# Performance work log

Measured on AMD Instinct MI355X. Metric: run time of the kernel, lower is better.

Reference implementation:

```python
import jax, jax.numpy as jnp
import numpy as np

N_NODES = 50000
N_EDGES = 800000
D_IN, D_HID, N_CLS, N_PROT = 128, 256, 16, 512
EPS = 1e-6


def setup_inputs() -> dict:
    key = jax.random.key(0)
    ks = jax.random.split(key, 12)
    s = 0.05
    return {
        "x": jax.random.normal(ks[0], (N_NODES, D_IN), dtype=jnp.float32),
        "edge_index": jax.random.randint(ks[1], (2, N_EDGES), 0, N_NODES, dtype=jnp.int64),
        "prot": jax.random.randint(ks[2], (N_PROT,), 0, N_NODES, dtype=jnp.int64),
        "epoch": 1,
        "W0": jax.random.normal(ks[3], (D_IN, D_HID), dtype=jnp.float32) * s,
        "b0": jnp.zeros((D_HID,), jnp.float32),
        "W1": jax.random.normal(ks[4], (D_HID, D_HID), dtype=jnp.float32) * s,
        "b1": jnp.zeros((D_HID,), jnp.float32),
        "Wl1": jax.random.normal(ks[5], (D_HID, D_HID), dtype=jnp.float32) * s,
        "bl1": jnp.zeros((D_HID,), jnp.float32),
        "Wl2": jax.random.normal(ks[6], (D_HID, N_CLS), dtype=jnp.float32) * s,
        "bl2": jnp.zeros((N_CLS,), jnp.float32),
    }


def _gcn_layer(h, W, b, src, dst, norm, n):
    # PyG GCNConv: h' = scatter_add(norm * (h @ W)[src] -> dst) + b
    m = (h @ W)[src] * norm[:, None]
    return jax.ops.segment_sum(m, dst, num_segments=n) + b


def _forward(x, edge_index, prot, W0, b0, W1, b1, Wl1, bl1, Wl2, bl2):
    n = x.shape[0]
    loops = jnp.arange(n, dtype=edge_index.dtype)
    src = jnp.concatenate([edge_index[0], loops])
    dst = jnp.concatenate([edge_index[1], loops])
    deg = jax.ops.segment_sum(jnp.ones_like(dst, dtype=x.dtype), dst, num_segments=n)
    dis = jax.lax.rsqrt(deg)  # deg >= 1 thanks to self loops
    norm = dis[src] * dis[dst]

    h = jax.nn.relu(_gcn_layer(x, W0, b0, src, dst, norm, n))
    h = _gcn_layer(h, W1, b1, src, dst, norm, n)

    # L2 row-normalize (torch divides by the norm directly)
    qn = jnp.linalg.norm(h, axis=1, keepdims=True)
    h = h / qn

    # relative_rep: cosine similarity of every node to each anchor
    anchors = h[prot]                             # [P, H]
    nx = jnp.linalg.norm(h, axis=1)               # [N]
    na = jnp.linalg.norm(anchors, axis=1)         # [P]
    num = h @ anchors.T                           # [N, P]
    x_rel = num / jnp.maximum(nx[:, None] * na[None, :], EPS)

    # classifier head on prototypes -> out_proto, then composed prediction
    lin = lambda z: jax.nn.relu(z @ Wl1 + bl1) @ Wl2 + bl2
    out_proto = jax.nn.log_softmax(lin(anchors), axis=-1)   # [P, C]
    out = jax.nn.log_softmax(x_rel @ out_proto, axis=-1)    # [N, C]
    return out, x_rel, out_proto


def reference(x, edge_index, prot, epoch, W0, b0, W1, b1, Wl1, bl1, Wl2, bl2):
    # epoch >= first_step_epochs (=0) branch: inference-path composition
    return _forward(x, edge_index, prot, W0, b0, W1, b1, Wl1, bl1, Wl2, bl2)


if __name__ == "__main__":
    out, x_rel, out_proto = reference(**setup_inputs())
    print(out.shape, x_rel.shape, out_proto.shape)
```

## Files before the change

kernel.cpp:

```cpp
#include <hip/hip_runtime.h>
#include <hip/hip_bf16.h>
#include <math.h>

#define NN 50000
#define NP 50048
#define EE 800000
#define DIN 128
#define HID 256
#define NCLS 16
#define NPROT 512

typedef __attribute__((ext_vector_type(8))) short short8;
typedef __attribute__((ext_vector_type(4))) float f32x4;

__device__ inline unsigned short f2b(float f) {
    union { float f; unsigned u; } c; c.f = f;
    unsigned u = c.u;
    unsigned r = (u + 0x7FFFu + ((u >> 16) & 1u)) >> 16;
    return (unsigned short)r;
}
__device__ inline float b2f(unsigned short u) {
    union { unsigned u; float f; } c; c.u = ((unsigned)u) << 16; return c.f;
}

#define GL2LDS16(g, l)                                                              \
    __builtin_amdgcn_global_load_lds(                                               \
        (const __attribute__((address_space(1))) unsigned int*)(g),                 \
        (__attribute__((address_space(3))) unsigned int*)(l), 16, 0, 0)


__global__ __launch_bounds__(256) void k_count(const int* __restrict__ dst, int* __restrict__ cnt, int e) {
    int i = blockIdx.x * 256 + threadIdx.x;
    if (i < e) atomicAdd(&cnt[dst[i]], 1);
}

__global__ __launch_bounds__(256) void k_scan1(const int* __restrict__ cnt, int* __restrict__ excl,
                                               int* __restrict__ bsum, float* __restrict__ dis, int n) {
    __shared__ int s[256];
    int t = threadIdx.x;
    int i = blockIdx.x * 256 + t;
    int v = (i < n) ? cnt[i] : 0;
    if (i < n) dis[i] = rsqrtf((float)v + 1.0f);
    s[t] = v; __syncthreads();
    for (int d = 1; d < 256; d <<= 1) {
        int add = (t >= d) ? s[t - d] : 0;
        __syncthreads();
        s[t] += add;
        __syncthreads();
    }
    if (i < n) excl[i] = s[t] - v;
    if (t == 255) bsum[blockIdx.x] = s[255];
}

__global__ __launch_bounds__(256) void k_scan2(const int* __restrict__ bsum, int* __restrict__ boff, int nb) {
    __shared__ int s[256];
    int t = threadIdx.x;
    int v = (t < nb) ? bsum[t] : 0;
    s[t] = v; __syncthreads();
    for (int d = 1; d < 256; d <<= 1) {
        int add = (t >= d) ? s[t - d] : 0;
        __syncthreads();
        s[t] += add;
        __syncthreads();
    }
    if (t < nb) boff[t] = s[t] - v;
}

__global__ __launch_bounds__(256) void k_scan3(const int* __restrict__ excl, const int* __restrict__ boff,
                                               int* __restrict__ off, int n, int e) {
    int i = blockIdx.x * 256 + threadIdx.x;
    if (i < n) off[i] = excl[i] + boff[blockIdx.x];
    if (i == 0) off[n] = e;
}

__global__ __launch_bounds__(256) void k_fill(const int* __restrict__ src, const int* __restrict__ dst,
                                              const int* __restrict__ off, int* __restrict__ cursor,
                                              const float* __restrict__ dis,
                                              int2* __restrict__ csr_e, int e) {
    int i = blockIdx.x * 256 + threadIdx.x;
    if (i >= e) return;
    int s = src[i], d = dst[i];
    int pos = atomicAdd(&cursor[d], 1);
    csr_e[off[d] + pos] = make_int2(s, __float_as_int(dis[s] * dis[d]));
}


#define CAST_BLKS (NN * DIN / 4 / 256)
#define WT0_BLKS  (DIN * HID / 256)
#define WT1_BLKS  (HID * HID / 256)

__global__ __launch_bounds__(256) void k_prep(const float* __restrict__ x, unsigned short* __restrict__ xb,
                                              const float* __restrict__ W0, unsigned short* __restrict__ Wt0,
                                              const float* __restrict__ W1, unsigned short* __restrict__ Wt1) {
    int b = blockIdx.x, t = threadIdx.x;
    if (b < CAST_BLKS) {
        int i = b * 256 + t;
        float4 v = ((const float4*)x)[i];
        ushort4 o; o.x = f2b(v.x); o.y = f2b(v.y); o.z = f2b(v.z); o.w = f2b(v.w);
        ((ushort4*)xb)[i] = o;
    } else if (b < CAST_BLKS + WT0_BLKS) {
        int i = (b - CAST_BLKS) * 256 + t;
        int k = i / HID, n = i - k * HID;
        Wt0[n * DIN + k] = f2b(W0[(size_t)k * HID + n]);
    } else {
        int i = (b - CAST_BLKS - WT0_BLKS) * 256 + t;
        int k = i / HID, n = i - k * HID;
        Wt1[n * HID + k] = f2b(W1[(size_t)k * HID + n]);
    }
}


__global__ __launch_bounds__(256) void k_gemm_mfma(const unsigned short* __restrict__ A,
                                                   const unsigned short* __restrict__ Bt,
                                                   void* __restrict__ C, int M, int Nc, int K, int mode,
                                                   const float* __restrict__ bias) {
    __shared__ __align__(16) unsigned short As[128 * 32];
    __shared__ __align__(16) unsigned short Bs[128 * 32];
    const int t = threadIdx.x;
    const int lane = t & 63;
    const int quad = lane >> 4;
    const int l16 = lane & 15;
    const int wv = t >> 6;
    const int wm = (wv & 1) * 64, wn = (wv >> 1) * 64;
    const int m0 = blockIdx.y * 128, n0 = blockIdx.x * 128;

    f32x4 acc[4][4];
#pragma unroll
    for (int i = 0; i < 4; ++i)
#pragma unroll
        for (int j = 0; j < 4; ++j)
#pragma unroll
            for (int r = 0; r < 4; ++r) acc[i][j][r] = 0.0f;

    const int sr = t >> 2;
    const int sc = (t & 3) * 8;

    for (int k0 = 0; k0 < K; k0 += 32) {
        GL2LDS16(A + (size_t)(m0 + sr) * K + k0 + sc,       &As[t * 8]);
        GL2LDS16(A + (size_t)(m0 + 64 + sr) * K + k0 + sc,  &As[2048 + t * 8]);
        GL2LDS16(Bt + (size_t)(n0 + sr) * K + k0 + sc,      &Bs[t * 8]);
        GL2LDS16(Bt + (size_t)(n0 + 64 + sr) * K + k0 + sc, &Bs[2048 + t * 8]);
        __syncthreads();
        short8 af[4], bf[4];
#pragma unroll
        for (int i = 0; i < 4; ++i)
            af[i] = *(const short8*)&As[(wm + i * 16 + l16) * 32 + quad * 8];
#pragma unroll
        for (int j = 0; j < 4; ++j)
            bf[j] = *(const short8*)&Bs[(wn + j * 16 + l16) * 32 + quad * 8];
#pragma unroll
        for (int i = 0; i < 4; ++i)
#pragma unroll
            for (int j = 0; j < 4; ++j)
                acc[i][j] = __builtin_amdgcn_mfma_f32_16x16x32_bf16(af[i], bf[j], acc[i][j], 0, 0, 0);
        __syncthreads();
    }

#pragma unroll
    for (int i = 0; i < 4; ++i) {
        int rb = m0 + wm + i * 16 + quad * 4;
#pragma unroll
        for (int j = 0; j < 4; ++j) {
            int col = n0 + wn + j * 16 + l16;
#pragma unroll
            for (int rg = 0; rg < 4; ++rg) {
                int r = rb + rg;
                float v = acc[i][j][rg];
                if (mode == 0) {
                    ((unsigned short*)C)[(size_t)r * Nc + col] = f2b(v);
                } else {
                    v = fmaxf(v + bias[col], 0.0f);
                    ((unsigned short*)C)[(size_t)r * Nc + col] = f2b(v);
                }
            }
        }
    }
}


__global__ __launch_bounds__(256) void k_agg128(const unsigned short* __restrict__ xw, const int* __restrict__ off,
                                                const int2* __restrict__ csr, const float* __restrict__ dis,
                                                unsigned short* __restrict__ out, int n) {
    int node = (blockIdx.x * 256 + threadIdx.x) >> 6;
    int lane = threadIdx.x & 63;
    if (node >= n) return;
    float d = dis[node];
    float w0 = d * d;
    ushort2 u = ((const ushort2*)(xw + (size_t)node * DIN))[lane];
    float a0 = w0 * b2f(u.x), a1 = w0 * b2f(u.y);
    int p = off[node], p1 = off[node + 1];
#define G128(e)                                                           \
    {                                                                     \
        ushort2 v = ((const ushort2*)(xw + (size_t)(e).x * DIN))[lane];   \
        float w = __int_as_float((e).y);                                  \
        a0 = fmaf(w, b2f(v.x), a0); a1 = fmaf(w, b2f(v.y), a1);           \
    }
    for (; p + 3 < p1; p += 4) {
        int2 e0 = csr[p], e1 = csr[p + 1], e2 = csr[p + 2], e3 = csr[p + 3];
        G128(e0) G128(e1) G128(e2) G128(e3)
    }
    for (; p < p1; ++p) { int2 e0 = csr[p]; G128(e0) }
#undef G128
    ushort2 o; o.x = f2b(a0); o.y = f2b(a1);
    ((ushort2*)(out + (size_t)node * DIN))[lane] = o;
}


__global__ __launch_bounds__(256) void k_agg256(const unsigned short* __restrict__ xw, const int* __restrict__ off,
                                                const int2* __restrict__ csr, const float* __restrict__ dis,
                                                const float* __restrict__ bias,
                                                unsigned short* __restrict__ out, float* __restrict__ nx, int n) {
    int node = (blockIdx.x * 256 + threadIdx.x) >> 6;
    int lane = threadIdx.x & 63;
    if (node >= n) return;
    float d = dis[node];
    float w0 = d * d;
    ushort4 u = ((const ushort4*)(xw + (size_t)node * HID))[lane];
    float a0 = w0 * b2f(u.x), a1 = w0 * b2f(u.y), a2 = w0 * b2f(u.z), a3 = w0 * b2f(u.w);
    int p = off[node], p1 = off[node + 1];
#define G256(e)                                                           \
    {                                                                     \
        ushort4 v = ((const ushort4*)(xw + (size_t)(e).x * HID))[lane];   \
        float w = __int_as_float((e).y);                                  \
        a0 = fmaf(w, b2f(v.x), a0); a1 = fmaf(w, b2f(v.y), a1);           \
        a2 = fmaf(w, b2f(v.z), a2); a3 = fmaf(w, b2f(v.w), a3);           \
    }
    for (; p + 3 < p1; p += 4) {
        int2 e0 = csr[p], e1 = csr[p + 1], e2 = csr[p + 2], e3 = csr[p + 3];
        G256(e0) G256(e1) G256(e2) G256(e3)
    }
    for (; p < p1; ++p) { int2 e0 = csr[p]; G256(e0) }
#undef G256
    float4 b = ((const float4*)bias)[lane];
    a0 += b.x; a1 += b.y; a2 += b.z; a3 += b.w;
    float ss = a0 * a0 + a1 * a1 + a2 * a2 + a3 * a3;
    for (int m = 32; m >= 1; m >>= 1) ss += __shfl_xor(ss, m, 64);
    float qn = sqrtf(ss);
    a0 /= qn; a1 /= qn; a2 /= qn; a3 /= qn;
    float s2 = a0 * a0 + a1 * a1 + a2 * a2 + a3 * a3;
    for (int m = 32; m >= 1; m >>= 1) s2 += __shfl_xor(s2, m, 64);
    if (lane == 0) nx[node] = sqrtf(s2);
    ushort4 o; o.x = f2b(a0); o.y = f2b(a1); o.z = f2b(a2); o.w = f2b(a3);
    ((ushort4*)(out + (size_t)node * HID))[lane] = o;
}


__global__ __launch_bounds__(256) void k_gproto(const unsigned short* __restrict__ hb,
                                                const int* __restrict__ prot, const float* __restrict__ nx,
                                                unsigned short* __restrict__ aRb, float* __restrict__ na,
                                                const float* __restrict__ Wl1, const float* __restrict__ bl1,
                                                const float* __restrict__ Wl2, const float* __restrict__ bl2,
                                                float* __restrict__ outp) {
    __shared__ float sa[HID];
    __shared__ float st[HID];
    int row = blockIdx.x, t = threadIdx.x;
    int p = prot[row];
    unsigned short us = hb[(size_t)p * HID + t];
    aRb[(size_t)row * HID + t] = us;
    sa[t] = b2f(us);
    if (t == 0) na[row] = nx[p];
    __syncthreads();
    float acc = bl1[t];
#pragma unroll 8
    for (int k = 0; k < HID; ++k) acc = fmaf(sa[k], Wl1[k * HID + t], acc);
    st[t] = fmaxf(acc, 0.0f);
    __syncthreads();
    if (t < 64) {
        int c = t & 15, ch = t >> 4;
        float z = 0.f;
#pragma unroll 8
        for (int k = ch * 64; k < ch * 64 + 64; ++k) z = fmaf(st[k], Wl2[k * NCLS + c], z);
        z += __shfl_xor(z, 16, 64);
        z += __shfl_xor(z, 32, 64);
        z += bl2[c];
        float m = z;
        for (int d = 8; d >= 1; d >>= 1) m = fmaxf(m, __shfl_xor(m, d, 64));
        float e = expf(z - m);
        float s = e;
        for (int d = 8; d >= 1; d >>= 1) s += __shfl_xor(s, d, 64);
        if (t < 16) outp[row * NCLS + c] = z - m - logf(s);
    }
}


#define XSW(row, cs) (((cs) ^ (((row) & 7) << 3)))
#define NWGX (4 * (NP / 128))

__global__ __launch_bounds__(256, 3) void k_xrel_out(const unsigned short* __restrict__ A,
                                                     const unsigned short* __restrict__ Bt,
                                                     const float* __restrict__ nx, const float* __restrict__ na,
                                                     const float* __restrict__ proto,
                                                     float* __restrict__ xrel, float* __restrict__ opart) {
    __shared__ __align__(16) unsigned short As[128 * 32];
    __shared__ __align__(16) unsigned short Bs[128 * 32];
    __shared__ __align__(16) unsigned short Xs[128 * 128];
    __shared__ __align__(16) unsigned short pTc[16 * 136];

    const int bid = blockIdx.x;
    const int q = NWGX / 8, r = NWGX % 8;
    const int xcd = bid & 7, li = bid >> 3;
    const int wk = (xcd < r ? xcd * (q + 1) : r * (q + 1) + (xcd - r) * q) + li;
    const int m0 = (wk >> 2) * 128;
    const int nc = wk & 3;
    const int n0 = nc * 128;

    const int t = threadIdx.x;
    const int lane = t & 63;
    const int quad = lane >> 4;
    const int l16 = lane & 15;
    const int wv = t >> 6;
    const int wm = (wv & 1) * 64, wn = (wv >> 1) * 64;

    float nxv[4][4];
#pragma unroll
    for (int i = 0; i < 4; ++i)
#pragma unroll
        for (int rg = 0; rg < 4; ++rg) {
            int rr = m0 + wm + i * 16 + quad * 4 + rg;
            nxv[i][rg] = nx[rr < NN ? rr : NN - 1];
        }
    float nav[4];
#pragma unroll
    for (int j = 0; j < 4; ++j) nav[j] = na[n0 + wn + j * 16 + l16];

    const int sr = t >> 2;
    const int sc = (t & 3) * 8;

    f32x4 acc[4][4];
#pragma unroll
    for (int i = 0; i < 4; ++i)
#pragma unroll
        for (int j = 0; j < 4; ++j)
#pragma unroll
            for (int rr = 0; rr < 4; ++rr) acc[i][j][rr] = 0.0f;

    for (int k0 = 0; k0 < HID; k0 += 32) {
        GL2LDS16(A + (size_t)(m0 + sr) * HID + k0 + sc,       &As[t * 8]);
        GL2LDS16(A + (size_t)(m0 + 64 + sr) * HID + k0 + sc,  &As[2048 + t * 8]);
        GL2LDS16(Bt + (size_t)(n0 + sr) * HID + k0 + sc,      &Bs[t * 8]);
        GL2LDS16(Bt + (size_t)(n0 + 64 + sr) * HID + k0 + sc, &Bs[2048 + t * 8]);
        __syncthreads();
        short8 af[4], bf[4];
#pragma unroll
        for (int i = 0; i < 4; ++i)
            af[i] = *(const short8*)&As[(wm + i * 16 + l16) * 32 + quad * 8];
#pragma unroll
        for (int j = 0; j < 4; ++j)
            bf[j] = *(const short8*)&Bs[(wn + j * 16 + l16) * 32 + quad * 8];
#pragma unroll
        for (int i = 0; i < 4; ++i)
#pragma unroll
            for (int j = 0; j < 4; ++j)
                acc[i][j] = __builtin_amdgcn_mfma_f32_16x16x32_bf16(af[i], bf[j], acc[i][j], 0, 0, 0);
        __syncthreads();
    }

    for (int i = t; i < 128 * NCLS; i += 256) {
        int kk = i >> 4, c = i & 15;
        pTc[c * 136 + kk] = f2b(proto[(n0 + kk) * NCLS + c]);
    }

#pragma unroll
    for (int i = 0; i < 4; ++i) {
#pragma unroll
        for (int j = 0; j < 4; ++j) {
            int cl = wn + j * 16 + l16;
#pragma unroll
            for (int rg = 0; rg < 4; ++rg) {
                int row = wm + i * 16 + quad * 4 + rg;
                float s = fmaxf(nxv[i][rg] * nav[j], 1e-6f);
                float v = acc[i][j][rg] * __builtin_amdgcn_rcpf(s);
                Xs[row * 128 + XSW(row, cl)] = f2b(v);
            }
        }
    }
    __syncthreads();

    f32x4 oacc[2];
#pragma unroll
    for (int rr = 0; rr < 4; ++rr) { oacc[0][rr] = 0.0f; oacc[1][rr] = 0.0f; }
#pragma unroll
    for (int ii = 0; ii < 2; ++ii) {
        int rb = wv * 32 + ii * 16;
#pragma unroll
        for (int ks = 0; ks < 4; ++ks) {
            int row = rb + l16;
            short8 af = *(const short8*)&Xs[row * 128 + XSW(row, ks * 32 + quad * 8)];
            short8 pb = *(const short8*)&pTc[l16 * 136 + ks * 32 + quad * 8];
            oacc[ii] = __builtin_amdgcn_mfma_f32_16x16x32_bf16(af, pb, oacc[ii], 0, 0, 0);
        }
    }
#pragma unroll
    for (int ii = 0; ii < 2; ++ii)
#pragma unroll
        for (int rg = 0; rg < 4; ++rg) {
            int lrow = wv * 32 + ii * 16 + quad * 4 + rg;
            opart[((size_t)nc * NP + m0 + lrow) * NCLS + l16] = oacc[ii][rg];
        }

#pragma unroll
    for (int it = 0; it < 8; ++it) {
        int idx = it * 256 + t;
        int row = idx >> 4;
        int c8 = (idx & 15) * 8;
        int rr = m0 + row;
        if (rr < NN) {
            short8 u = *(const short8*)&Xs[row * 128 + XSW(row, c8)];
            float* dst = &xrel[(size_t)rr * NPROT + n0 + c8];
            float4 v0, v1;
            v0.x = b2f((unsigned short)u[0]); v0.y = b2f((unsigned short)u[1]);
            v0.z = b2f((unsigned short)u[2]); v0.w = b2f((unsigned short)u[3]);
            v1.x = b2f((unsigned short)u[4]); v1.y = b2f((unsigned short)u[5]);
            v1.z = b2f((unsigned short)u[6]); v1.w = b2f((unsigned short)u[7]);
            *(float4*)dst = v0;
            *(float4*)(dst + 4) = v1;
        }
    }
}


__global__ __launch_bounds__(256) void k_reduce(const float* __restrict__ opart, float* __restrict__ out) {
    int i = blockIdx.x * 256 + threadIdx.x;
    int row = i >> 4, c = i & 15;
    float z = opart[i] + opart[(size_t)NP * NCLS + i] + opart[(size_t)2 * NP * NCLS + i] +
              opart[(size_t)3 * NP * NCLS + i];
    float mx = z;
    for (int d = 8; d >= 1; d >>= 1) mx = fmaxf(mx, __shfl_xor(mx, d, 64));
    float e = expf(z - mx);
    float s = e;
    for (int d = 8; d >= 1; d >>= 1) s += __shfl_xor(s, d, 64);
    if (row < NN) out[(size_t)row * NCLS + c] = z - mx - logf(s);
}


extern "C" void kernel_launch(void* const* d_in, const int* in_sizes, int n_in,
                              void* d_out, int out_size, void* d_ws, size_t ws_size,
                              hipStream_t stream) {
    const float* x    = (const float*)d_in[0];
    const int*   eidx = (const int*)d_in[1];
    const int*   prot = (const int*)d_in[2];
    const float* W0  = (const float*)d_in[4];
    const float* b0  = (const float*)d_in[5];
    const float* W1  = (const float*)d_in[6];
    const float* b1  = (const float*)d_in[7];
    const float* Wl1 = (const float*)d_in[8];
    const float* bl1 = (const float*)d_in[9];
    const float* Wl2 = (const float*)d_in[10];
    const float* bl2 = (const float*)d_in[11];

    const int N = NN, E = EE;
    const int* esrc_in = eidx;
    const int* edst_in = eidx + E;

    float* out_final = (float*)d_out;
    float* x_rel     = (float*)d_out + (size_t)N * NCLS;
    float* out_proto = x_rel + (size_t)N * NPROT;

    char* w = (char*)d_ws;
    auto alloc = [&](size_t bytes) { char* p = w; w += (bytes + 255) & ~(size_t)255; return p; };
    int*   cnt      = (int*)alloc((size_t)N * 4);
    int*   cursor   = (int*)alloc((size_t)N * 4);
    float* dis      = (float*)alloc((size_t)N * 4);
    int*   excl     = (int*)alloc((size_t)N * 4);
    int*   csr_off  = (int*)alloc((size_t)(N + 1) * 4);
    int*   bsum     = (int*)alloc(1024);
    int*   boff     = (int*)alloc(1024);
    int2*  csr_e    = (int2*)alloc((size_t)E * 8);
    float* nx       = (float*)alloc((size_t)N * 4);
    float* na       = (float*)alloc((size_t)NPROT * 4);
    float* opart    = (float*)alloc((size_t)4 * NP * NCLS * 4);
    unsigned short* xb    = (unsigned short*)alloc((size_t)NP * DIN * 2);
    unsigned short* Wt0   = (unsigned short*)alloc((size_t)HID * DIN * 2);
    unsigned short* Wt1   = (unsigned short*)alloc((size_t)HID * HID * 2);
    unsigned short* bufAb = (unsigned short*)alloc((size_t)NP * HID * 2);
    unsigned short* h0b   = (unsigned short*)alloc((size_t)NP * HID * 2);
    unsigned short* aRb   = (unsigned short*)alloc((size_t)NPROT * HID * 2);
    unsigned short* a1 = bufAb;
    unsigned short* hb = h0b;

    hipMemsetAsync(cnt, 0, (size_t)N * 4, stream);
    hipMemsetAsync(cursor, 0, (size_t)N * 4, stream);

    k_count<<<(E + 255) / 256, 256, 0, stream>>>(edst_in, cnt, E);
    int NB = (N + 255) / 256;
    k_scan1<<<NB, 256, 0, stream>>>(cnt, excl, bsum, dis, N);
    k_scan2<<<1, 256, 0, stream>>>(bsum, boff, NB);
    k_scan3<<<NB, 256, 0, stream>>>(excl, boff, csr_off, N, E);
    k_fill<<<(E + 255) / 256, 256, 0, stream>>>(esrc_in, edst_in, csr_off, cursor, dis, csr_e, E);

    k_prep<<<CAST_BLKS + WT0_BLKS + WT1_BLKS, 256, 0, stream>>>(x, xb, W0, Wt0, W1, Wt1);

    const int MT = NP / 128;

    k_agg128<<<(N + 3) / 4, 256, 0, stream>>>(xb, csr_off, csr_e, dis, a1, N);
    k_gemm_mfma<<<dim3(HID / 128, MT), 256, 0, stream>>>(a1, Wt0, h0b, N, HID, DIN, 2, b0);

    k_gemm_mfma<<<dim3(HID / 128, MT), 256, 0, stream>>>(h0b, Wt1, bufAb, N, HID, HID, 0, nullptr);
    k_agg256<<<(N + 3) / 4, 256, 0, stream>>>(bufAb, csr_off, csr_e, dis, b1, hb, nx, N);

    k_gproto<<<NPROT, 256, 0, stream>>>(hb, prot, nx, aRb, na, Wl1, bl1, Wl2, bl2, out_proto);

    k_xrel_out<<<NWGX, 256, 0, stream>>>(hb, aRb, nx, na, out_proto, x_rel, opart);

    k_reduce<<<NP * NCLS / 256, 256, 0, stream>>>(opart, out_final);
}
```

Baseline: 447.1 us.

## Pad CSR rows to multiples of eight and unroll aggregation by eight

Each node's CSR segment is rounded up to a multiple of 8 entries, zero-filled (src 0, weight 0), so the aggregation loops can read edges as aligned int4 pairs and issue eight gathers per iteration with no remainder loop. Launch bounds hint occupancy 4. The cost is extra memset of the padded edge buffer and wasted gathers of node 0 for padding entries, about 44% more gather work in the worst case.

```diff
diff --git a/kernel.cpp b/kernel.cpp
--- a/kernel.cpp
+++ b/kernel.cpp
@@ -5,6 +5,7 @@
 #define NN 50000
 #define NP 50048
 #define EE 800000
+#define EPAD 1150016
 #define DIN 128
 #define HID 256
 #define NCLS 16
@@ -41,14 +42,15 @@
     int i = blockIdx.x * 256 + t;
     int v = (i < n) ? cnt[i] : 0;
     if (i < n) dis[i] = rsqrtf((float)v + 1.0f);
-    s[t] = v; __syncthreads();
+    int vp = (v + 7) & ~7;
+    s[t] = vp; __syncthreads();
     for (int d = 1; d < 256; d <<= 1) {
         int add = (t >= d) ? s[t - d] : 0;
         __syncthreads();
         s[t] += add;
         __syncthreads();
     }
-    if (i < n) excl[i] = s[t] - v;
+    if (i < n) excl[i] = s[t] - vp;
     if (t == 255) bsum[blockIdx.x] = s[255];
 }
 
@@ -67,10 +69,11 @@
 }
 
 __global__ __launch_bounds__(256) void k_scan3(const int* __restrict__ excl, const int* __restrict__ boff,
-                                               int* __restrict__ off, int n, int e) {
+                                               const int* __restrict__ bsum,
+                                               int* __restrict__ off, int n, int nb) {
     int i = blockIdx.x * 256 + threadIdx.x;
     if (i < n) off[i] = excl[i] + boff[blockIdx.x];
-    if (i == 0) off[n] = e;
+    if (i == 0) off[n] = boff[nb - 1] + bsum[nb - 1];
 }
 
 __global__ __launch_bounds__(256) void k_fill(const int* __restrict__ src, const int* __restrict__ dst,
@@ -178,9 +181,9 @@
 }
 
 
-__global__ __launch_bounds__(256) void k_agg128(const unsigned short* __restrict__ xw, const int* __restrict__ off,
-                                                const int2* __restrict__ csr, const float* __restrict__ dis,
-                                                unsigned short* __restrict__ out, int n) {
+__global__ __launch_bounds__(256, 4) void k_agg128(const unsigned short* __restrict__ xw, const int* __restrict__ off,
+                                                   const int2* __restrict__ csr, const float* __restrict__ dis,
+                                                   unsigned short* __restrict__ out, int n) {
     int node = (blockIdx.x * 256 + threadIdx.x) >> 6;
     int lane = threadIdx.x & 63;
     if (node >= n) return;
@@ -189,27 +192,38 @@
     ushort2 u = ((const ushort2*)(xw + (size_t)node * DIN))[lane];
     float a0 = w0 * b2f(u.x), a1 = w0 * b2f(u.y);
     int p = off[node], p1 = off[node + 1];
-#define G128(e)                                                           \
-    {                                                                     \
-        ushort2 v = ((const ushort2*)(xw + (size_t)(e).x * DIN))[lane];   \
-        float w = __int_as_float((e).y);                                  \
-        a0 = fmaf(w, b2f(v.x), a0); a1 = fmaf(w, b2f(v.y), a1);           \
-    }
-    for (; p + 3 < p1; p += 4) {
-        int2 e0 = csr[p], e1 = csr[p + 1], e2 = csr[p + 2], e3 = csr[p + 3];
-        G128(e0) G128(e1) G128(e2) G128(e3)
-    }
-    for (; p < p1; ++p) { int2 e0 = csr[p]; G128(e0) }
-#undef G128
+    for (; p < p1; p += 8) {
+        int4 dA = *(const int4*)(csr + p);
+        int4 dB = *(const int4*)(csr + p + 2);
+        int4 dC = *(const int4*)(csr + p + 4);
+        int4 dD = *(const int4*)(csr + p + 6);
+        ushort2 v0 = ((const ushort2*)(xw + (size_t)dA.x * DIN))[lane];
+        ushort2 v1 = ((const ushort2*)(xw + (size_t)dA.z * DIN))[lane];
+        ushort2 v2 = ((const ushort2*)(xw + (size_t)dB.x * DIN))[lane];
+        ushort2 v3 = ((const ushort2*)(xw + (size_t)dB.z * DIN))[lane];
+        ushort2 v4 = ((const ushort2*)(xw + (size_t)dC.x * DIN))[lane];
+        ushort2 v5 = ((const ushort2*)(xw + (size_t)dC.z * DIN))[lane];
+        ushort2 v6 = ((const ushort2*)(xw + (size_t)dD.x * DIN))[lane];
+        ushort2 v7 = ((const ushort2*)(xw + (size_t)dD.z * DIN))[lane];
+        float w;
+        w = __int_as_float(dA.y); a0 = fmaf(w, b2f(v0.x), a0); a1 = fmaf(w, b2f(v0.y), a1);
+        w = __int_as_float(dA.w); a0 = fmaf(w, b2f(v1.x), a0); a1 = fmaf(w, b2f(v1.y), a1);
+        w = __int_as_float(dB.y); a0 = fmaf(w, b2f(v2.x), a0); a1 = fmaf(w, b2f(v2.y), a1);
+        w = __int_as_float(dB.w); a0 = fmaf(w, b2f(v3.x), a0); a1 = fmaf(w, b2f(v3.y), a1);
+        w = __int_as_float(dC.y); a0 = fmaf(w, b2f(v4.x), a0); a1 = fmaf(w, b2f(v4.y), a1);
+        w = __int_as_float(dC.w); a0 = fmaf(w, b2f(v5.x), a0); a1 = fmaf(w, b2f(v5.y), a1);
+        w = __int_as_float(dD.y); a0 = fmaf(w, b2f(v6.x), a0); a1 = fmaf(w, b2f(v6.y), a1);
+        w = __int_as_float(dD.w); a0 = fmaf(w, b2f(v7.x), a0); a1 = fmaf(w, b2f(v7.y), a1);
+    }
     ushort2 o; o.x = f2b(a0); o.y = f2b(a1);
     ((ushort2*)(out + (size_t)node * DIN))[lane] = o;
 }
 
 
-__global__ __launch_bounds__(256) void k_agg256(const unsigned short* __restrict__ xw, const int* __restrict__ off,
-                                                const int2* __restrict__ csr, const float* __restrict__ dis,
-                                                const float* __restrict__ bias,
-                                                unsigned short* __restrict__ out, float* __restrict__ nx, int n) {
+__global__ __launch_bounds__(256, 4) void k_agg256(const unsigned short* __restrict__ xw, const int* __restrict__ off,
+                                                   const int2* __restrict__ csr, const float* __restrict__ dis,
+                                                   const float* __restrict__ bias,
+                                                   unsigned short* __restrict__ out, float* __restrict__ nx, int n) {
     int node = (blockIdx.x * 256 + threadIdx.x) >> 6;
     int lane = threadIdx.x & 63;
     if (node >= n) return;
@@ -218,19 +232,37 @@
     ushort4 u = ((const ushort4*)(xw + (size_t)node * HID))[lane];
     float a0 = w0 * b2f(u.x), a1 = w0 * b2f(u.y), a2 = w0 * b2f(u.z), a3 = w0 * b2f(u.w);
     int p = off[node], p1 = off[node + 1];
-#define G256(e)                                                           \
-    {                                                                     \
-        ushort4 v = ((const ushort4*)(xw + (size_t)(e).x * HID))[lane];   \
-        float w = __int_as_float((e).y);                                  \
-        a0 = fmaf(w, b2f(v.x), a0); a1 = fmaf(w, b2f(v.y), a1);           \
-        a2 = fmaf(w, b2f(v.z), a2); a3 = fmaf(w, b2f(v.w), a3);           \
-    }
-    for (; p + 3 < p1; p += 4) {
-        int2 e0 = csr[p], e1 = csr[p + 1], e2 = csr[p + 2], e3 = csr[p + 3];
-        G256(e0) G256(e1) G256(e2) G256(e3)
-    }
-    for (; p < p1; ++p) { int2 e0 = csr[p]; G256(e0) }
-#undef G256
+    for (; p < p1; p += 8) {
+        int4 dA = *(const int4*)(csr + p);
+        int4 dB = *(const int4*)(csr + p + 2);
+        int4 dC = *(const int4*)(csr + p + 4);
+        int4 dD = *(const int4*)(csr + p + 6);
+        ushort4 v0 = ((const ushort4*)(xw + (size_t)dA.x * HID))[lane];
+        ushort4 v1 = ((const ushort4*)(xw + (size_t)dA.z * HID))[lane];
+        ushort4 v2 = ((const ushort4*)(xw + (size_t)dB.x * HID))[lane];
+        ushort4 v3 = ((const ushort4*)(xw + (size_t)dB.z * HID))[lane];
+        ushort4 v4 = ((const ushort4*)(xw + (size_t)dC.x * HID))[lane];
+        ushort4 v5 = ((const ushort4*)(xw + (size_t)dC.z * HID))[lane];
+        ushort4 v6 = ((const ushort4*)(xw + (size_t)dD.x * HID))[lane];
+        ushort4 v7 = ((const ushort4*)(xw + (size_t)dD.z * HID))[lane];
+        float w;
+        w = __int_as_float(dA.y);
+        a0 = fmaf(w, b2f(v0.x), a0); a1 = fmaf(w, b2f(v0.y), a1); a2 = fmaf(w, b2f(v0.z), a2); a3 = fmaf(w, b2f(v0.w), a3);
+        w = __int_as_float(dA.w);
+        a0 = fmaf(w, b2f(v1.x), a0); a1 = fmaf(w, b2f(v1.y), a1); a2 = fmaf(w, b2f(v1.z), a2); a3 = fmaf(w, b2f(v1.w), a3);
+        w = __int_as_float(dB.y);
+        a0 = fmaf(w, b2f(v2.x), a0); a1 = fmaf(w, b2f(v2.y), a1); a2 = fmaf(w, b2f(v2.z), a2); a3 = fmaf(w, b2f(v2.w), a3);
+        w = __int_as_float(dB.w);
+        a0 = fmaf(w, b2f(v3.x), a0); a1 = fmaf(w, b2f(v3.y), a1); a2 = fmaf(w, b2f(v3.z), a2); a3 = fmaf(w, b2f(v3.w), a3);
+        w = __int_as_float(dC.y);
+        a0 = fmaf(w, b2f(v4.x), a0); a1 = fmaf(w, b2f(v4.y), a1); a2 = fmaf(w, b2f(v4.z), a2); a3 = fmaf(w, b2f(v4.w), a3);
+        w = __int_as_float(dC.w);
+        a0 = fmaf(w, b2f(v5.x), a0); a1 = fmaf(w, b2f(v5.y), a1); a2 = fmaf(w, b2f(v5.z), a2); a3 = fmaf(w, b2f(v5.w), a3);
+        w = __int_as_float(dD.y);
+        a0 = fmaf(w, b2f(v6.x), a0); a1 = fmaf(w, b2f(v6.y), a1); a2 = fmaf(w, b2f(v6.z), a2); a3 = fmaf(w, b2f(v6.w), a3);
+        w = __int_as_float(dD.w);
+        a0 = fmaf(w, b2f(v7.x), a0); a1 = fmaf(w, b2f(v7.y), a1); a2 = fmaf(w, b2f(v7.z), a2); a3 = fmaf(w, b2f(v7.w), a3);
+    }
     float4 b = ((const float4*)bias)[lane];
     a0 += b.x; a1 += b.y; a2 += b.z; a3 += b.w;
     float ss = a0 * a0 + a1 * a1 + a2 * a2 + a3 * a3;
@@ -465,7 +497,7 @@
     int*   csr_off  = (int*)alloc((size_t)(N + 1) * 4);
     int*   bsum     = (int*)alloc(1024);
     int*   boff     = (int*)alloc(1024);
-    int2*  csr_e    = (int2*)alloc((size_t)E * 8);
+    int2*  csr_e    = (int2*)alloc((size_t)EPAD * 8);
     float* nx       = (float*)alloc((size_t)N * 4);
     float* na       = (float*)alloc((size_t)NPROT * 4);
     float* opart    = (float*)alloc((size_t)4 * NP * NCLS * 4);
@@ -480,12 +512,13 @@
 
     hipMemsetAsync(cnt, 0, (size_t)N * 4, stream);
     hipMemsetAsync(cursor, 0, (size_t)N * 4, stream);
+    hipMemsetAsync(csr_e, 0, (size_t)EPAD * 8, stream);
 
     k_count<<<(E + 255) / 256, 256, 0, stream>>>(edst_in, cnt, E);
     int NB = (N + 255) / 256;
     k_scan1<<<NB, 256, 0, stream>>>(cnt, excl, bsum, dis, N);
     k_scan2<<<1, 256, 0, stream>>>(bsum, boff, NB);
-    k_scan3<<<NB, 256, 0, stream>>>(excl, boff, csr_off, N, E);
+    k_scan3<<<NB, 256, 0, stream>>>(excl, boff, bsum, csr_off, N, NB);
     k_fill<<<(E + 255) / 256, 256, 0, stream>>>(esrc_in, edst_in, csr_off, cursor, dis, csr_e, E);
 
     k_prep<<<CAST_BLKS + WT0_BLKS + WT1_BLKS, 256, 0, stream>>>(x, xb, W0, Wt0, W1, Wt1);
```

Result: no change. 441.5 us (-1.2%).

## Stage neighbor gathers through LDS with padded CSR and shrink xrel LDS

Applied to the files above, without the earlier changes.

Both GCN aggregation kernels now load edge indices and weights once per wave into registers and spread them with shuffles. They then gather up to 32 or 16 neighbor rows at a time into per-wave LDS buffers using global_load_lds, waiting on the whole batch before accumulating. The goal is more memory loads in flight than the previous four-edge unrolled register loop. CSR rows are padded to multiples of 8 with zeroed entries, which costs an extra memset and some wasted gathers of row 0 with zero weight. The xrel/out kernel also overlays its GEMM staging buffers onto the Xs tile so it can raise launch_bounds occupancy from 3 to 4 blocks.

```diff
diff --git a/kernel.cpp b/kernel.cpp
--- a/kernel.cpp
+++ b/kernel.cpp
@@ -5,6 +5,7 @@
 #define NN 50000
 #define NP 50048
 #define EE 800000
+#define EPAD 1150016
 #define DIN 128
 #define HID 256
 #define NCLS 16
@@ -41,14 +42,15 @@
     int i = blockIdx.x * 256 + t;
     int v = (i < n) ? cnt[i] : 0;
     if (i < n) dis[i] = rsqrtf((float)v + 1.0f);
-    s[t] = v; __syncthreads();
+    int vp = (v + 7) & ~7;
+    s[t] = vp; __syncthreads();
     for (int d = 1; d < 256; d <<= 1) {
         int add = (t >= d) ? s[t - d] : 0;
         __syncthreads();
         s[t] += add;
         __syncthreads();
     }
-    if (i < n) excl[i] = s[t] - v;
+    if (i < n) excl[i] = s[t] - vp;
     if (t == 255) bsum[blockIdx.x] = s[255];
 }
 
@@ -67,10 +69,11 @@
 }
 
 __global__ __launch_bounds__(256) void k_scan3(const int* __restrict__ excl, const int* __restrict__ boff,
-                                               int* __restrict__ off, int n, int e) {
+                                               const int* __restrict__ bsum,
+                                               int* __restrict__ off, int n, int nb) {
     int i = blockIdx.x * 256 + threadIdx.x;
     if (i < n) off[i] = excl[i] + boff[blockIdx.x];
-    if (i == 0) off[n] = e;
+    if (i == 0) off[n] = boff[nb - 1] + bsum[nb - 1];
 }
 
 __global__ __launch_bounds__(256) void k_fill(const int* __restrict__ src, const int* __restrict__ dst,
@@ -181,26 +184,37 @@
 __global__ __launch_bounds__(256) void k_agg128(const unsigned short* __restrict__ xw, const int* __restrict__ off,
                                                 const int2* __restrict__ csr, const float* __restrict__ dis,
                                                 unsigned short* __restrict__ out, int n) {
+    __shared__ __align__(16) unsigned short rb[4 * 32 * 128];
     int node = (blockIdx.x * 256 + threadIdx.x) >> 6;
     int lane = threadIdx.x & 63;
+    unsigned short* mybuf = rb + (threadIdx.x >> 6) * (32 * 128);
     if (node >= n) return;
     float d = dis[node];
     float w0 = d * d;
     ushort2 u = ((const ushort2*)(xw + (size_t)node * DIN))[lane];
     float a0 = w0 * b2f(u.x), a1 = w0 * b2f(u.y);
     int p = off[node], p1 = off[node + 1];
-#define G128(e)                                                           \
-    {                                                                     \
-        ushort2 v = ((const ushort2*)(xw + (size_t)(e).x * DIN))[lane];   \
-        float w = __int_as_float((e).y);                                  \
-        a0 = fmaf(w, b2f(v.x), a0); a1 = fmaf(w, b2f(v.y), a1);           \
-    }
-    for (; p + 3 < p1; p += 4) {
-        int2 e0 = csr[p], e1 = csr[p + 1], e2 = csr[p + 2], e3 = csr[p + 3];
-        G128(e0) G128(e1) G128(e2) G128(e3)
-    }
-    for (; p < p1; ++p) { int2 e0 = csr[p]; G128(e0) }
-#undef G128
+    while (p < p1) {
+        int seg = min(p1 - p, 64);
+        int2 di = csr[p + (lane < seg ? lane : seg - 1)];
+        for (int b = 0; b < seg; b += 32) {
+            int nrows = min(32, seg - b);
+            for (int s = 0; s < nrows; s += 4) {
+                int e = b + s + ((lane >> 4) & 3);
+                int srcn = __shfl(di.x, e, 64);
+                GL2LDS16(xw + (size_t)srcn * DIN + (lane & 15) * 8, &mybuf[s * 128]);
+            }
+            asm volatile("s_waitcnt vmcnt(0)" ::: "memory");
+            __builtin_amdgcn_sched_barrier(0);
+            for (int k = 0; k < nrows; ++k) {
+                float w = __int_as_float(__shfl(di.y, b + k, 64));
+                ushort2 v = *(const ushort2*)&mybuf[k * 128 + lane * 2];
+                a0 = fmaf(w, b2f(v.x), a0); a1 = fmaf(w, b2f(v.y), a1);
+            }
+            __builtin_amdgcn_sched_barrier(0);
+        }
+        p += seg;
+    }
     ushort2 o; o.x = f2b(a0); o.y = f2b(a1);
     ((ushort2*)(out + (size_t)node * DIN))[lane] = o;
 }
@@ -210,27 +224,38 @@
                                                 const int2* __restrict__ csr, const float* __restrict__ dis,
                                                 const float* __restrict__ bias,
                                                 unsigned short* __restrict__ out, float* __restrict__ nx, int n) {
+    __shared__ __align__(16) unsigned short rb[4 * 16 * 256];
     int node = (blockIdx.x * 256 + threadIdx.x) >> 6;
     int lane = threadIdx.x & 63;
+    unsigned short* mybuf = rb + (threadIdx.x >> 6) * (16 * 256);
     if (node >= n) return;
     float d = dis[node];
     float w0 = d * d;
     ushort4 u = ((const ushort4*)(xw + (size_t)node * HID))[lane];
     float a0 = w0 * b2f(u.x), a1 = w0 * b2f(u.y), a2 = w0 * b2f(u.z), a3 = w0 * b2f(u.w);
     int p = off[node], p1 = off[node + 1];
-#define G256(e)                                                           \
-    {                                                                     \
-        ushort4 v = ((const ushort4*)(xw + (size_t)(e).x * HID))[lane];   \
-        float w = __int_as_float((e).y);                                  \
-        a0 = fmaf(w, b2f(v.x), a0); a1 = fmaf(w, b2f(v.y), a1);           \
-        a2 = fmaf(w, b2f(v.z), a2); a3 = fmaf(w, b2f(v.w), a3);           \
-    }
-    for (; p + 3 < p1; p += 4) {
-        int2 e0 = csr[p], e1 = csr[p + 1], e2 = csr[p + 2], e3 = csr[p + 3];
-        G256(e0) G256(e1) G256(e2) G256(e3)
-    }
-    for (; p < p1; ++p) { int2 e0 = csr[p]; G256(e0) }
-#undef G256
+    while (p < p1) {
+        int seg = min(p1 - p, 64);
+        int2 di = csr[p + (lane < seg ? lane : seg - 1)];
+        for (int b = 0; b < seg; b += 16) {
+            int nrows = min(16, seg - b);
+            for (int s = 0; s < nrows; s += 2) {
+                int e = b + s + (lane >> 5);
+                int srcn = __shfl(di.x, e, 64);
+                GL2LDS16(xw + (size_t)srcn * HID + (lane & 31) * 8, &mybuf[s * 256]);
+            }
+            asm volatile("s_waitcnt vmcnt(0)" ::: "memory");
+            __builtin_amdgcn_sched_barrier(0);
+            for (int k = 0; k < nrows; ++k) {
+                float w = __int_as_float(__shfl(di.y, b + k, 64));
+                ushort4 v = *(const ushort4*)&mybuf[k * 256 + lane * 4];
+                a0 = fmaf(w, b2f(v.x), a0); a1 = fmaf(w, b2f(v.y), a1);
+                a2 = fmaf(w, b2f(v.z), a2); a3 = fmaf(w, b2f(v.w), a3);
+            }
+            __builtin_amdgcn_sched_barrier(0);
+        }
+        p += seg;
+    }
     float4 b = ((const float4*)bias)[lane];
     a0 += b.x; a1 += b.y; a2 += b.z; a3 += b.w;
     float ss = a0 * a0 + a1 * a1 + a2 * a2 + a3 * a3;
@@ -286,15 +311,12 @@
 #define XSW(row, cs) (((cs) ^ (((row) & 7) << 3)))
 #define NWGX (4 * (NP / 128))
 
-__global__ __launch_bounds__(256, 3) void k_xrel_out(const unsigned short* __restrict__ A,
+__global__ __launch_bounds__(256, 4) void k_xrel_out(const unsigned short* __restrict__ A,
                                                      const unsigned short* __restrict__ Bt,
                                                      const float* __restrict__ nx, const float* __restrict__ na,
                                                      const float* __restrict__ proto,
                                                      float* __restrict__ xrel, float* __restrict__ opart) {
-    __shared__ __align__(16) unsigned short As[128 * 32];
-    __shared__ __align__(16) unsigned short Bs[128 * 32];
-    __shared__ __align__(16) unsigned short Xs[128 * 128];
-    __shared__ __align__(16) unsigned short pTc[16 * 136];
+    __shared__ __align__(16) unsigned short smem_us[18560];
 
     const int bid = blockIdx.x;
     const int q = NWGX / 8, r = NWGX % 8;
@@ -335,18 +357,18 @@
             for (int rr = 0; rr < 4; ++rr) acc[i][j][rr] = 0.0f;
 
     for (int k0 = 0; k0 < HID; k0 += 32) {
-        GL2LDS16(A + (size_t)(m0 + sr) * HID + k0 + sc,       &As[t * 8]);
-        GL2LDS16(A + (size_t)(m0 + 64 + sr) * HID + k0 + sc,  &As[2048 + t * 8]);
-        GL2LDS16(Bt + (size_t)(n0 + sr) * HID + k0 + sc,      &Bs[t * 8]);
-        GL2LDS16(Bt + (size_t)(n0 + 64 + sr) * HID + k0 + sc, &Bs[2048 + t * 8]);
+        GL2LDS16(A + (size_t)(m0 + sr) * HID + k0 + sc,        &smem_us[t * 8]);
+        GL2LDS16(A + (size_t)(m0 + 64 + sr) * HID + k0 + sc,   &smem_us[2048 + t * 8]);
+        GL2LDS16(Bt + (size_t)(n0 + sr) * HID + k0 + sc,       &smem_us[4096 + t * 8]);
+        GL2LDS16(Bt + (size_t)(n0 + 64 + sr) * HID + k0 + sc,  &smem_us[4096 + 2048 + t * 8]);
         __syncthreads();
         short8 af[4], bf[4];
 #pragma unroll
         for (int i = 0; i < 4; ++i)
-            af[i] = *(const short8*)&As[(wm + i * 16 + l16) * 32 + quad * 8];
+            af[i] = *(const short8*)&smem_us[(wm + i * 16 + l16) * 32 + quad * 8];
 #pragma unroll
         for (int j = 0; j < 4; ++j)
-            bf[j] = *(const short8*)&Bs[(wn + j * 16 + l16) * 32 + quad * 8];
+            bf[j] = *(const short8*)&smem_us[4096 + (wn + j * 16 + l16) * 32 + quad * 8];
 #pragma unroll
         for (int i = 0; i < 4; ++i)
 #pragma unroll
@@ -357,7 +379,7 @@
 
     for (int i = t; i < 128 * NCLS; i += 256) {
         int kk = i >> 4, c = i & 15;
-        pTc[c * 136 + kk] = f2b(proto[(n0 + kk) * NCLS + c]);
+        smem_us[16384 + c * 136 + kk] = f2b(proto[(n0 + kk) * NCLS + c]);
     }
 
 #pragma unroll
@@ -370,7 +392,7 @@
                 int row = wm + i * 16 + quad * 4 + rg;
                 float s = fmaxf(nxv[i][rg] * nav[j], 1e-6f);
                 float v = acc[i][j][rg] * __builtin_amdgcn_rcpf(s);
-                Xs[row * 128 + XSW(row, cl)] = f2b(v);
+                smem_us[row * 128 + XSW(row, cl)] = f2b(v);
             }
         }
     }
@@ -381,12 +403,12 @@
     for (int rr = 0; rr < 4; ++rr) { oacc[0][rr] = 0.0f; oacc[1][rr] = 0.0f; }
 #pragma unroll
     for (int ii = 0; ii < 2; ++ii) {
-        int rb = wv * 32 + ii * 16;
+        int rbr = wv * 32 + ii * 16;
 #pragma unroll
         for (int ks = 0; ks < 4; ++ks) {
-            int row = rb + l16;
-            short8 af = *(const short8*)&Xs[row * 128 + XSW(row, ks * 32 + quad * 8)];
-            short8 pb = *(const short8*)&pTc[l16 * 136 + ks * 32 + quad * 8];
+            int row = rbr + l16;
+            short8 af = *(const short8*)&smem_us[row * 128 + XSW(row, ks * 32 + quad * 8)];
+            short8 pb = *(const short8*)&smem_us[16384 + l16 * 136 + ks * 32 + quad * 8];
             oacc[ii] = __builtin_amdgcn_mfma_f32_16x16x32_bf16(af, pb, oacc[ii], 0, 0, 0);
         }
     }
@@ -405,7 +427,7 @@
         int c8 = (idx & 15) * 8;
         int rr = m0 + row;
         if (rr < NN) {
-            short8 u = *(const short8*)&Xs[row * 128 + XSW(row, c8)];
+            short8 u = *(const short8*)&smem_us[row * 128 + XSW(row, c8)];
             float* dst = &xrel[(size_t)rr * NPROT + n0 + c8];
             float4 v0, v1;
             v0.x = b2f((unsigned short)u[0]); v0.y = b2f((unsigned short)u[1]);
@@ -465,7 +487,7 @@
     int*   csr_off  = (int*)alloc((size_t)(N + 1) * 4);
     int*   bsum     = (int*)alloc(1024);
     int*   boff     = (int*)alloc(1024);
-    int2*  csr_e    = (int2*)alloc((size_t)E * 8);
+    int2*  csr_e    = (int2*)alloc((size_t)EPAD * 8);
     float* nx       = (float*)alloc((size_t)N * 4);
     float* na       = (float*)alloc((size_t)NPROT * 4);
     float* opart    = (float*)alloc((size_t)4 * NP * NCLS * 4);
@@ -480,12 +502,13 @@
 
     hipMemsetAsync(cnt, 0, (size_t)N * 4, stream);
     hipMemsetAsync(cursor, 0, (size_t)N * 4, stream);
+    hipMemsetAsync(csr_e, 0, (size_t)EPAD * 8, stream);
 
     k_count<<<(E + 255) / 256, 256, 0, stream>>>(edst_in, cnt, E);
     int NB = (N + 255) / 256;
     k_scan1<<<NB, 256, 0, stream>>>(cnt, excl, bsum, dis, N);
     k_scan2<<<1, 256, 0, stream>>>(bsum, boff, NB);
-    k_scan3<<<NB, 256, 0, stream>>>(excl, boff, csr_off, N, E);
+    k_scan3<<<NB, 256, 0, stream>>>(excl, boff, bsum, csr_off, N, NB);
     k_fill<<<(E + 255) / 256, 256, 0, stream>>>(esrc_in, edst_in, csr_off, cursor, dis, csr_e, E);
 
     k_prep<<<CAST_BLKS + WT0_BLKS + WT1_BLKS, 256, 0, stream>>>(x, xb, W0, Wt0, W1, Wt1);
```

Measured after the change: 464.1 us. 3.8% more time.
